# Kernel tuning notes

Measured on AMD Instinct MI355X. Metric: run time of the kernel, lower is better.

## Reference

```python
import jax, jax.numpy as jnp
import numpy as np

K = 20          # neighbors per centroid
OUT_CH = 256    # out_channel
EPS = 1e-5      # batchnorm eps


def _bn(x, gamma, beta, axes):
    # batch-norm in training mode (batch statistics), per-channel on last axis
    mu = jnp.mean(x, axis=axes, keepdims=True)
    var = jnp.var(x, axis=axes, keepdims=True)
    return (x - mu) * jax.lax.rsqrt(var + EPS) * gamma + beta


def _forward(centroid, xyz, radius, dist,
             w_xyz, b_xyz, g0, be0, w1, g1, be1, w2, g2, be2):
    B, N, _ = xyz.shape
    M = centroid.shape[1]
    # --- sample_and_group: radius mask + index sort + gather ---
    ar = jnp.arange(N, dtype=jnp.int32)                       # [N]
    idx = jnp.where(dist > radius, N, ar[None, None, :])      # [B,M,N]
    idx = jnp.sort(idx, axis=-1)[:, :, :K]                    # [B,M,K] lowest in-radius indices
    first = idx[:, :, :1]
    idx = jnp.where(idx == N, first, idx)                     # pad with first neighbor
    pf = jax.vmap(lambda f, i: f[i])(xyz, idx)                # [B,M,K,3] gather
    # --- concat (points, neighbors, variance) -> 9 channels ---
    pts = jnp.broadcast_to(centroid[:, :, None, :], (B, M, K, 3))
    feat = jnp.concatenate([pts, pf, pf - pts], axis=-1)      # [B,M,K,9]
    # --- 1x1 conv2d + BN2d + GELU (exact erf, as torch nn.GELU) ---
    h = jnp.einsum('bmkc,oc->bmko', feat, w_xyz) + b_xyz      # [B,M,K,C/8]
    h = jax.nn.gelu(_bn(h, g0, be0, axes=(0, 1, 2)), approximate=False)
    # --- max over k neighbors ---
    h = jnp.max(h, axis=2)                                    # [B,M,C/8]
    # --- MLP: Conv1x1 (no bias) + BN1d + GELU, then Conv1x1 + BN1d ---
    h = jnp.einsum('bmc,oc->bmo', h, w1)
    h = jax.nn.gelu(_bn(h, g1, be1, axes=(0, 1)), approximate=False)
    h = jnp.einsum('bmc,oc->bmo', h, w2)
    h = _bn(h, g2, be2, axes=(0, 1))                          # [B,M,OUT_CH]
    return h


def setup_inputs() -> dict:
    key = jax.random.key(0)
    ks = jax.random.split(key, 10)
    B, M, N = 4, 2048, 8192
    c8, c4 = OUT_CH // 8, OUT_CH // 4
    return {
        'centroid': jax.random.uniform(ks[0], (B, M, 3), jnp.float32),
        'xyz': jax.random.uniform(ks[1], (B, N, 3), jnp.float32),
        'radius': jax.random.uniform(ks[2], (B, M, 1), jnp.float32),
        'dist': jax.random.uniform(ks[3], (B, M, N), jnp.float32),
        'w_xyz': jax.random.normal(ks[4], (c8, 9), jnp.float32) * 0.3,
        'b_xyz': jnp.zeros((c8,), jnp.float32),
        'g0': jnp.ones((c8,), jnp.float32),
        'be0': jnp.zeros((c8,), jnp.float32),
        'w1': jax.random.normal(ks[5], (c4, c8), jnp.float32) * 0.2,
        'g1': jnp.ones((c4,), jnp.float32),
        'be1': jnp.zeros((c4,), jnp.float32),
        'w2': jax.random.normal(ks[6], (OUT_CH, c4), jnp.float32) * 0.15,
        'g2': jnp.ones((OUT_CH,), jnp.float32),
        'be2': jnp.zeros((OUT_CH,), jnp.float32),
    }


def reference(centroid, xyz, radius, dist, w_xyz, b_xyz, g0, be0,
              w1, g1, be1, w2, g2, be2):
    return _forward(centroid, xyz, radius, dist, w_xyz, b_xyz, g0, be0,
                    w1, g1, be1, w2, g2, be2)
```

## Files before the change

kernel.cpp:

```cpp
#include <hip/hip_runtime.h>
#include <cstdint>
#include <cstddef>

#define K_NB   20
#define N_PTS  8192
#define M_CENT 2048
#define B_SZ   4
#define C8     32
#define C4     64
#define COUT   256
#define EPSV   1e-5f
#define NROWS  (B_SZ * M_CENT)

#define NP0 64
#define NP1 32
#define NP2 16

__device__ __forceinline__ float gelu_exact(float x) {
    return 0.5f * x * (1.0f + erff(x * 0.7071067811865476f));
}

__global__ __launch_bounds__(256) void k_select_mlp0(
    const float* __restrict__ centroid, const float* __restrict__ xyz,
    const float* __restrict__ radius,   const float* __restrict__ dist,
    const float* __restrict__ w_xyz,    const float* __restrict__ b_xyz,
    float* __restrict__ h0,
    double* __restrict__ p0sum, double* __restrict__ p0sq)
{
    __shared__ int   idx_sh[4][K_NB];
    __shared__ float ss[256], qq[256];
    const int tid  = threadIdx.x;
    const int wave = tid >> 6;
    const int lane = tid & 63;
    const int row  = blockIdx.x * 4 + wave;
    const int b    = row >> 11;
    const float rad = radius[row];
    const float* drow = dist + (size_t)row * N_PTS;

    int cnt = 0;
    for (int base = 0; base < N_PTS && cnt < K_NB; base += 256) {
        const float4 v = reinterpret_cast<const float4*>(drow + base)[lane];
        unsigned mloc = (v.x <= rad ? 1u : 0u) | (v.y <= rad ? 2u : 0u)
                      | (v.z <= rad ? 4u : 0u) | (v.w <= rad ? 8u : 0u);
        uint64_t b0 = __ballot(mloc & 1u);
        uint64_t b1 = __ballot(mloc & 2u);
        uint64_t b2 = __ballot(mloc & 4u);
        uint64_t b3 = __ballot(mloc & 8u);
        uint64_t lt = (1ull << lane) - 1ull;
        int r = __popcll(b0 & lt) + __popcll(b1 & lt)
              + __popcll(b2 & lt) + __popcll(b3 & lt);
        const int myidx = base + lane * 4;
        if (mloc & 1u) { int p = cnt + r; if (p < K_NB) idx_sh[wave][p] = myidx + 0; r++; }
        if (mloc & 2u) { int p = cnt + r; if (p < K_NB) idx_sh[wave][p] = myidx + 1; r++; }
        if (mloc & 4u) { int p = cnt + r; if (p < K_NB) idx_sh[wave][p] = myidx + 2; r++; }
        if (mloc & 8u) { int p = cnt + r; if (p < K_NB) idx_sh[wave][p] = myidx + 3; r++; }
        cnt += __popcll(b0) + __popcll(b1) + __popcll(b2) + __popcll(b3);
    }
    __syncthreads();

    const int cfill = (cnt < K_NB) ? cnt : K_NB;
    const int fillv = (cnt == 0) ? (N_PTS - 1) : idx_sh[wave][0];
    if (lane < K_NB && lane >= cfill) idx_sh[wave][lane] = fillv;
    __syncthreads();

    const int ch = lane & 31;
    const int kk = lane >> 5;
    const float* w = w_xyz + ch * 9;
    const float wc0 = w[0] - w[6], wc1 = w[1] - w[7], wc2 = w[2] - w[8];
    const float wp0 = w[3] + w[6], wp1 = w[4] + w[7], wp2 = w[5] + w[8];
    const float bias = b_xyz[ch];
    const float cx = centroid[row * 3 + 0];
    const float cy = centroid[row * 3 + 1];
    const float cz = centroid[row * 3 + 2];
    const float cterm = bias + cx * wc0 + cy * wc1 + cz * wc2;

    float* hrow = h0 + (size_t)row * K_NB * C8;
    float s = 0.f, q = 0.f;
    #pragma unroll
    for (int t = 0; t < 10; t++) {
        const int k = 2 * t + kk;
        const int idx = idx_sh[wave][k];
        const float* p = xyz + ((size_t)b * N_PTS + idx) * 3;
        const float h = cterm + p[0] * wp0 + p[1] * wp1 + p[2] * wp2;
        hrow[k * C8 + ch] = h;
        s += h; q += h * h;
    }

    ss[tid] = s; qq[tid] = q;
    __syncthreads();
    if (tid < C8) {
        float S = 0.f, Q = 0.f;
        #pragma unroll
        for (int r = 0; r < 8; r++) { S += ss[tid + 32 * r]; Q += qq[tid + 32 * r]; }
        const int part = blockIdx.x & (NP0 - 1);
        atomicAdd(&p0sum[part * C8 + tid], (double)S);
        atomicAdd(&p0sq [part * C8 + tid], (double)Q);
    }
}

__global__ __launch_bounds__(256) void k_bn0_max_mm1(
    const float* __restrict__ h0,
    const double* __restrict__ p0sum, const double* __restrict__ p0sq,
    const float* __restrict__ g0, const float* __restrict__ be0,
    const float* __restrict__ w1, float* __restrict__ h1,
    double* __restrict__ p1sum, double* __restrict__ p1sq)
{
    __shared__ float sc[C8], sh[C8];
    __shared__ float w1s[C4 * C8];
    __shared__ float a_sh[4][C8];
    __shared__ float r1[4][C4];
    const int tid = threadIdx.x;
    if (tid < C8) {
        double S = 0.0, Q = 0.0;
        #pragma unroll 8
        for (int p = 0; p < NP0; p++) { S += p0sum[p * C8 + tid]; Q += p0sq[p * C8 + tid]; }
        const double inv = 1.0 / (double)((long)NROWS * K_NB);
        const double mu  = S * inv;
        const double var = Q * inv - mu * mu;
        const float sf = g0[tid] / sqrtf((float)var + EPSV);
        sc[tid] = sf;
        sh[tid] = be0[tid] - (float)mu * sf;
    }
    for (int i = tid; i < C4 * C8; i += 256) w1s[i] = w1[i];
    __syncthreads();

    const int wave = tid >> 6, lane = tid & 63;
    const int row  = blockIdx.x * 4 + wave;
    const int ch   = lane & 31, kk = lane >> 5;
    const float s = sc[ch], b = sh[ch];
    const float* hrow = h0 + (size_t)row * K_NB * C8;
    float mx = -3.0e38f;
    #pragma unroll
    for (int t = 0; t < 10; t++) {
        const int k = 2 * t + kk;
        const float y = gelu_exact(hrow[k * C8 + ch] * s + b);
        mx = fmaxf(mx, y);
    }
    mx = fmaxf(mx, __shfl_xor(mx, 32));
    if (lane < 32) a_sh[wave][lane] = mx;
    __syncthreads();

    float acc = 0.f;
    #pragma unroll
    for (int c = 0; c < C8; c++) acc += a_sh[wave][c] * w1s[lane * C8 + c];
    h1[(size_t)row * C4 + lane] = acc;

    r1[wave][lane] = acc;
    __syncthreads();
    if (tid < C4) {
        const float v0 = r1[0][tid], v1 = r1[1][tid], v2 = r1[2][tid], v3 = r1[3][tid];
        const float S = v0 + v1 + v2 + v3;
        const float Q = v0 * v0 + v1 * v1 + v2 * v2 + v3 * v3;
        const int part = blockIdx.x & (NP1 - 1);
        atomicAdd(&p1sum[part * C4 + tid], (double)S);
        atomicAdd(&p1sq [part * C4 + tid], (double)Q);
    }
}

__global__ __launch_bounds__(256) void k_bn1_mm2(
    const float* __restrict__ h1,
    const double* __restrict__ p1sum, const double* __restrict__ p1sq,
    const float* __restrict__ g1, const float* __restrict__ be1,
    const float* __restrict__ w2, float* __restrict__ h2,
    double* __restrict__ p2sum, double* __restrict__ p2sq)
{
    __shared__ float sc[C4], sh[C4];
    __shared__ float a_sh[4][C4];
    __shared__ float v2s[4][COUT];
    const int tid = threadIdx.x;
    if (tid < C4) {
        double S = 0.0, Q = 0.0;
        #pragma unroll 8
        for (int p = 0; p < NP1; p++) { S += p1sum[p * C4 + tid]; Q += p1sq[p * C4 + tid]; }
        const double inv = 1.0 / (double)NROWS;
        const double mu  = S * inv;
        const double var = Q * inv - mu * mu;
        const float sf = g1[tid] / sqrtf((float)var + EPSV);
        sc[tid] = sf;
        sh[tid] = be1[tid] - (float)mu * sf;
    }
    __syncthreads();

    const int wave = tid >> 6, lane = tid & 63;
    const int row  = blockIdx.x * 4 + wave;
    const float v  = h1[(size_t)row * C4 + lane];
    a_sh[wave][lane] = gelu_exact(v * sc[lane] + sh[lane]);
    __syncthreads();

    float acc0 = 0.f, acc1 = 0.f, acc2 = 0.f, acc3 = 0.f;
    #pragma unroll 8
    for (int c = 0; c < C4; c++) {
        const float a = a_sh[wave][c];
        acc0 += a * w2[(0 * 64 + lane) * C4 + c];
        acc1 += a * w2[(1 * 64 + lane) * C4 + c];
        acc2 += a * w2[(2 * 64 + lane) * C4 + c];
        acc3 += a * w2[(3 * 64 + lane) * C4 + c];
    }
    float* orow = h2 + (size_t)row * COUT;
    orow[0 * 64 + lane] = acc0;
    orow[1 * 64 + lane] = acc1;
    orow[2 * 64 + lane] = acc2;
    orow[3 * 64 + lane] = acc3;

    v2s[wave][0 * 64 + lane] = acc0;
    v2s[wave][1 * 64 + lane] = acc1;
    v2s[wave][2 * 64 + lane] = acc2;
    v2s[wave][3 * 64 + lane] = acc3;
    __syncthreads();
    {
        float S = 0.f, Q = 0.f;
        #pragma unroll
        for (int w = 0; w < 4; w++) { const float x = v2s[w][tid]; S += x; Q += x * x; }
        const int part = blockIdx.x & (NP2 - 1);
        atomicAdd(&p2sum[part * COUT + tid], (double)S);
        atomicAdd(&p2sq [part * COUT + tid], (double)Q);
    }
}

__global__ __launch_bounds__(256) void k_bn2_out(
    const float* __restrict__ h2,
    const double* __restrict__ p2sum, const double* __restrict__ p2sq,
    const float* __restrict__ g2, const float* __restrict__ be2,
    float* __restrict__ out)
{
    __shared__ float sc[COUT], sh[COUT];
    const int tid = threadIdx.x;
    {
        double S = 0.0, Q = 0.0;
        #pragma unroll
        for (int p = 0; p < NP2; p++) { S += p2sum[p * COUT + tid]; Q += p2sq[p * COUT + tid]; }
        const double inv = 1.0 / (double)NROWS;
        const double mu  = S * inv;
        const double var = Q * inv - mu * mu;
        const float sf = g2[tid] / sqrtf((float)var + EPSV);
        sc[tid] = sf;
        sh[tid] = be2[tid] - (float)mu * sf;
    }
    __syncthreads();
    const int total4 = NROWS * COUT / 4;
    for (int i = blockIdx.x * 256 + tid; i < total4; i += gridDim.x * 256) {
        const float4 v = reinterpret_cast<const float4*>(h2)[i];
        const int ch = (i * 4) & 255;
        float4 o;
        o.x = v.x * sc[ch + 0] + sh[ch + 0];
        o.y = v.y * sc[ch + 1] + sh[ch + 1];
        o.z = v.z * sc[ch + 2] + sh[ch + 2];
        o.w = v.w * sc[ch + 3] + sh[ch + 3];
        reinterpret_cast<float4*>(out)[i] = o;
    }
}

extern "C" void kernel_launch(void* const* d_in, const int* in_sizes, int n_in,
                              void* d_out, int out_size, void* d_ws, size_t ws_size,
                              hipStream_t stream) {
    const float* centroid = (const float*)d_in[0];
    const float* xyz      = (const float*)d_in[1];
    const float* radius   = (const float*)d_in[2];
    const float* dist     = (const float*)d_in[3];
    const float* w_xyz    = (const float*)d_in[4];
    const float* b_xyz    = (const float*)d_in[5];
    const float* g0       = (const float*)d_in[6];
    const float* be0      = (const float*)d_in[7];
    const float* w1       = (const float*)d_in[8];
    const float* g1       = (const float*)d_in[9];
    const float* be1      = (const float*)d_in[10];
    const float* w2       = (const float*)d_in[11];
    const float* g2       = (const float*)d_in[12];
    const float* be2      = (const float*)d_in[13];
    float* out = (float*)d_out;

    char* ws = (char*)d_ws;
    double* p0sum = (double*)ws;
    double* p0sq  = p0sum + NP0 * C8;
    double* p1sum = p0sq  + NP0 * C8;
    double* p1sq  = p1sum + NP1 * C4;
    double* p2sum = p1sq  + NP1 * C4;
    double* p2sq  = p2sum + NP2 * COUT;
    const size_t part_bytes = (size_t)(4 * NP0 * C8 + 2 * NP2 * COUT) * sizeof(double);
    float* h0 = (float*)(ws + 131072);
    float* h1 = h0 + (size_t)NROWS * K_NB * C8;
    float* h2 = h1 + (size_t)NROWS * C4;

    hipMemsetAsync(ws, 0, part_bytes, stream);

    k_select_mlp0<<<NROWS / 4, 256, 0, stream>>>(centroid, xyz, radius, dist,
                                                 w_xyz, b_xyz, h0, p0sum, p0sq);
    k_bn0_max_mm1<<<NROWS / 4, 256, 0, stream>>>(h0, p0sum, p0sq, g0, be0, w1,
                                                 h1, p1sum, p1sq);
    k_bn1_mm2<<<NROWS / 4, 256, 0, stream>>>(h1, p1sum, p1sq, g1, be1, w2,
                                             h2, p2sum, p2sq);
    k_bn2_out<<<512, 256, 0, stream>>>(h2, p2sum, p2sq, g2, be2, out);
}
```

Before: 440.2 us.

## Reduce per-neighbor activations to min/max before GELU and unroll distance scan

The first kernel now keeps only the per-channel min and max of the pre-BN activations over the K neighbors, instead of writing all K values to a workspace. The second kernel applies BN plus GELU to just those two values and takes their max. This is valid because BN is a per-channel affine map and GELU first decreases and then increases, so its maximum over a set lies at one of the extremes. The change removes a large intermediate write and read. The radius scan now issues four float4 loads per iteration to raise memory-level parallelism, at the cost of sometimes reading past where the neighbor search could stop. The memset that zeroed the partial-sum buffers was also removed, which risks accumulating stale statistics across calls unless they are reset elsewhere.

```diff
diff --git a/kernel.cpp b/kernel.cpp
--- a/kernel.cpp
+++ b/kernel.cpp
@@ -20,11 +20,11 @@
     return 0.5f * x * (1.0f + erff(x * 0.7071067811865476f));
 }
 
-__global__ __launch_bounds__(256) void k_select_mlp0(
+__global__ __launch_bounds__(256) void k_scan_mlp0(
     const float* __restrict__ centroid, const float* __restrict__ xyz,
     const float* __restrict__ radius,   const float* __restrict__ dist,
     const float* __restrict__ w_xyz,    const float* __restrict__ b_xyz,
-    float* __restrict__ h0,
+    float* __restrict__ hmin, float* __restrict__ hmax,
     double* __restrict__ p0sum, double* __restrict__ p0sq)
 {
     __shared__ int   idx_sh[4][K_NB];
@@ -38,23 +38,29 @@
     const float* drow = dist + (size_t)row * N_PTS;
 
     int cnt = 0;
-    for (int base = 0; base < N_PTS && cnt < K_NB; base += 256) {
-        const float4 v = reinterpret_cast<const float4*>(drow + base)[lane];
-        unsigned mloc = (v.x <= rad ? 1u : 0u) | (v.y <= rad ? 2u : 0u)
-                      | (v.z <= rad ? 4u : 0u) | (v.w <= rad ? 8u : 0u);
-        uint64_t b0 = __ballot(mloc & 1u);
-        uint64_t b1 = __ballot(mloc & 2u);
-        uint64_t b2 = __ballot(mloc & 4u);
-        uint64_t b3 = __ballot(mloc & 8u);
-        uint64_t lt = (1ull << lane) - 1ull;
-        int r = __popcll(b0 & lt) + __popcll(b1 & lt)
-              + __popcll(b2 & lt) + __popcll(b3 & lt);
-        const int myidx = base + lane * 4;
-        if (mloc & 1u) { int p = cnt + r; if (p < K_NB) idx_sh[wave][p] = myidx + 0; r++; }
-        if (mloc & 2u) { int p = cnt + r; if (p < K_NB) idx_sh[wave][p] = myidx + 1; r++; }
-        if (mloc & 4u) { int p = cnt + r; if (p < K_NB) idx_sh[wave][p] = myidx + 2; r++; }
-        if (mloc & 8u) { int p = cnt + r; if (p < K_NB) idx_sh[wave][p] = myidx + 3; r++; }
-        cnt += __popcll(b0) + __popcll(b1) + __popcll(b2) + __popcll(b3);
+    for (int base = 0; base < N_PTS && cnt < K_NB; base += 1024) {
+        float4 v[4];
+        #pragma unroll
+        for (int s = 0; s < 4; s++)
+            v[s] = reinterpret_cast<const float4*>(drow + base + s * 256)[lane];
+        #pragma unroll
+        for (int s = 0; s < 4; s++) {
+            unsigned mloc = (v[s].x <= rad ? 1u : 0u) | (v[s].y <= rad ? 2u : 0u)
+                          | (v[s].z <= rad ? 4u : 0u) | (v[s].w <= rad ? 8u : 0u);
+            uint64_t b0 = __ballot(mloc & 1u);
+            uint64_t b1 = __ballot(mloc & 2u);
+            uint64_t b2 = __ballot(mloc & 4u);
+            uint64_t b3 = __ballot(mloc & 8u);
+            uint64_t lt = (1ull << lane) - 1ull;
+            int r = __popcll(b0 & lt) + __popcll(b1 & lt)
+                  + __popcll(b2 & lt) + __popcll(b3 & lt);
+            const int myidx = base + s * 256 + lane * 4;
+            if (mloc & 1u) { int p = cnt + r; if (p < K_NB) idx_sh[wave][p] = myidx + 0; r++; }
+            if (mloc & 2u) { int p = cnt + r; if (p < K_NB) idx_sh[wave][p] = myidx + 1; r++; }
+            if (mloc & 4u) { int p = cnt + r; if (p < K_NB) idx_sh[wave][p] = myidx + 2; r++; }
+            if (mloc & 8u) { int p = cnt + r; if (p < K_NB) idx_sh[wave][p] = myidx + 3; r++; }
+            cnt += __popcll(b0) + __popcll(b1) + __popcll(b2) + __popcll(b3);
+        }
     }
     __syncthreads();
 
@@ -68,23 +74,23 @@
     const float* w = w_xyz + ch * 9;
     const float wc0 = w[0] - w[6], wc1 = w[1] - w[7], wc2 = w[2] - w[8];
     const float wp0 = w[3] + w[6], wp1 = w[4] + w[7], wp2 = w[5] + w[8];
-    const float bias = b_xyz[ch];
-    const float cx = centroid[row * 3 + 0];
-    const float cy = centroid[row * 3 + 1];
-    const float cz = centroid[row * 3 + 2];
-    const float cterm = bias + cx * wc0 + cy * wc1 + cz * wc2;
-
-    float* hrow = h0 + (size_t)row * K_NB * C8;
-    float s = 0.f, q = 0.f;
+    const float cterm = b_xyz[ch] + centroid[row * 3 + 0] * wc0
+                      + centroid[row * 3 + 1] * wc1
+                      + centroid[row * 3 + 2] * wc2;
+
+    float s = 0.f, q = 0.f, mn = 3.0e38f, mx = -3.0e38f;
     #pragma unroll
     for (int t = 0; t < 10; t++) {
-        const int k = 2 * t + kk;
-        const int idx = idx_sh[wave][k];
+        const int idx = idx_sh[wave][2 * t + kk];
         const float* p = xyz + ((size_t)b * N_PTS + idx) * 3;
         const float h = cterm + p[0] * wp0 + p[1] * wp1 + p[2] * wp2;
-        hrow[k * C8 + ch] = h;
         s += h; q += h * h;
-    }
+        mn = fminf(mn, h); mx = fmaxf(mx, h);
+    }
+    mn = fminf(mn, __shfl_xor(mn, 32));
+    mx = fmaxf(mx, __shfl_xor(mx, 32));
+    if (lane < 32) hmin[row * C8 + ch] = mn;
+    else           hmax[row * C8 + ch] = mx;
 
     ss[tid] = s; qq[tid] = q;
     __syncthreads();
@@ -99,7 +105,7 @@
 }
 
 __global__ __launch_bounds__(256) void k_bn0_max_mm1(
-    const float* __restrict__ h0,
+    const float* __restrict__ hmin, const float* __restrict__ hmax,
     const double* __restrict__ p0sum, const double* __restrict__ p0sq,
     const float* __restrict__ g0, const float* __restrict__ be0,
     const float* __restrict__ w1, float* __restrict__ h1,
@@ -108,7 +114,7 @@
     __shared__ float sc[C8], sh[C8];
     __shared__ float w1s[C4 * C8];
     __shared__ float a_sh[4][C8];
-    __shared__ float r1[4][C4];
+    __shared__ float r1s[4][C4];
     const int tid = threadIdx.x;
     if (tid < C8) {
         double S = 0.0, Q = 0.0;
@@ -126,18 +132,11 @@
 
     const int wave = tid >> 6, lane = tid & 63;
     const int row  = blockIdx.x * 4 + wave;
-    const int ch   = lane & 31, kk = lane >> 5;
-    const float s = sc[ch], b = sh[ch];
-    const float* hrow = h0 + (size_t)row * K_NB * C8;
-    float mx = -3.0e38f;
-    #pragma unroll
-    for (int t = 0; t < 10; t++) {
-        const int k = 2 * t + kk;
-        const float y = gelu_exact(hrow[k * C8 + ch] * s + b);
-        mx = fmaxf(mx, y);
-    }
-    mx = fmaxf(mx, __shfl_xor(mx, 32));
-    if (lane < 32) a_sh[wave][lane] = mx;
+    const int ch   = lane & 31;
+    const float v  = (lane < 32 ? hmin : hmax)[row * C8 + ch];
+    float ge = gelu_exact(v * sc[ch] + sh[ch]);
+    ge = fmaxf(ge, __shfl_xor(ge, 32));
+    if (lane < 32) a_sh[wave][lane] = ge;
     __syncthreads();
 
     float acc = 0.f;
@@ -145,10 +144,10 @@
     for (int c = 0; c < C8; c++) acc += a_sh[wave][c] * w1s[lane * C8 + c];
     h1[(size_t)row * C4 + lane] = acc;
 
-    r1[wave][lane] = acc;
+    r1s[wave][lane] = acc;
     __syncthreads();
     if (tid < C4) {
-        const float v0 = r1[0][tid], v1 = r1[1][tid], v2 = r1[2][tid], v3 = r1[3][tid];
+        const float v0 = r1s[0][tid], v1 = r1s[1][tid], v2 = r1s[2][tid], v3 = r1s[3][tid];
         const float S = v0 + v1 + v2 + v3;
         const float Q = v0 * v0 + v1 * v1 + v2 * v2 + v3 * v3;
         const int part = blockIdx.x & (NP1 - 1);
@@ -276,17 +275,16 @@
     double* p1sq  = p1sum + NP1 * C4;
     double* p2sum = p1sq  + NP1 * C4;
     double* p2sq  = p2sum + NP2 * COUT;
-    const size_t part_bytes = (size_t)(4 * NP0 * C8 + 2 * NP2 * COUT) * sizeof(double);
-    float* h0 = (float*)(ws + 131072);
-    float* h1 = h0 + (size_t)NROWS * K_NB * C8;
-    float* h2 = h1 + (size_t)NROWS * C4;
-
-    hipMemsetAsync(ws, 0, part_bytes, stream);
-
-    k_select_mlp0<<<NROWS / 4, 256, 0, stream>>>(centroid, xyz, radius, dist,
-                                                 w_xyz, b_xyz, h0, p0sum, p0sq);
-    k_bn0_max_mm1<<<NROWS / 4, 256, 0, stream>>>(h0, p0sum, p0sq, g0, be0, w1,
-                                                 h1, p1sum, p1sq);
+    float* hmin = (float*)(ws + 131072);
+    float* hmax = hmin + (size_t)NROWS * C8;
+    float* h1   = hmax + (size_t)NROWS * C8;
+    float* h2   = h1   + (size_t)NROWS * C4;
+
+    k_scan_mlp0<<<NROWS / 4, 256, 0, stream>>>(centroid, xyz, radius, dist,
+                                               w_xyz, b_xyz, hmin, hmax,
+                                               p0sum, p0sq);
+    k_bn0_max_mm1<<<NROWS / 4, 256, 0, stream>>>(hmin, hmax, p0sum, p0sq,
+                                                 g0, be0, w1, h1, p1sum, p1sq);
     k_bn1_mm2<<<NROWS / 4, 256, 0, stream>>>(h1, p1sum, p1sq, g1, be1, w2,
                                              h2, p2sum, p2sq);
     k_bn2_out<<<512, 256, 0, stream>>>(h2, p2sum, p2sq, g2, be2, out);
```

After: 419.6 us. 4.7% less time.
